# Kernel tuning notes

Hardware: AMD Instinct MI355X
Metric: run time of the kernel (lower is better)

The kernel has to match this reference:

```python
import jax, jax.numpy as jnp
import numpy as np

B, N, C = 8, 4096, 768
H = 12
D = C // H            # 64
BN = C // 2           # bottleneck dim 384
EPS_LN = 1e-5
EPS_ATTN = 1e-6


def layer_norm(x, g, b):
    mu = jnp.mean(x, axis=-1, keepdims=True)
    var = jnp.mean(jnp.square(x - mu), axis=-1, keepdims=True)
    return (x - mu) * jax.lax.rsqrt(var + EPS_LN) * g + b


def setup_inputs() -> dict:
    key = jax.random.key(0)
    ks = jax.random.split(key, 8)
    s = 0.02
    return {
        "x": jax.random.normal(ks[0], (B, N, C), jnp.float32),
        "w_qkv": jax.random.normal(ks[1], (C, 3 * C), jnp.float32) * s,
        "b_qkv": jnp.zeros((3 * C,), jnp.float32),
        "w_proj": jax.random.normal(ks[2], (C, C), jnp.float32) * s,
        "b_proj": jnp.zeros((C,), jnp.float32),
        "g1": jnp.ones((C,), jnp.float32),
        "beta1": jnp.zeros((C,), jnp.float32),
        "g2": jnp.ones((C,), jnp.float32),
        "beta2": jnp.zeros((C,), jnp.float32),
        "w_down": jax.random.normal(ks[3], (C, BN), jnp.float32) * s,
        "b_down": jnp.zeros((BN,), jnp.float32),
        "w_up": jax.random.normal(ks[4], (BN, C), jnp.float32) * s,
        "b_up": jnp.zeros((C,), jnp.float32),
        "g3": jnp.ones((C,), jnp.float32),
        "beta3": jnp.zeros((C,), jnp.float32),
    }


def _linear_attention(x, w_qkv, b_qkv, w_proj, b_proj):
    # x: (B, N, C)
    qkv = x @ w_qkv + b_qkv                       # (B, N, 3C)
    qkv = qkv.reshape(B, N, 3, H, D)
    qkv = jnp.transpose(qkv, (2, 0, 3, 1, 4))     # (3, B, H, N, D)
    q, k, v = qkv[0], qkv[1], qkv[2]
    fm = lambda t: jax.nn.elu(t) + 1.0            # positive feature map
    q, k = fm(q), fm(k)
    kv = jnp.einsum('bhnd,bhnv->bhdv', k, v)      # (B, H, D, D)
    out = jnp.einsum('bhnd,bhdv->bhnv', q, kv)    # (B, H, N, D)
    k_sum = k.sum(axis=2)                         # (B, H, D)
    normalizer = jnp.einsum('bhnd,bhd->bhn', q, k_sum) + EPS_ATTN
    out = out / normalizer[..., None]
    out = jnp.transpose(out, (0, 2, 1, 3)).reshape(B, N, C)
    return out @ w_proj + b_proj


def reference(x, w_qkv, b_qkv, w_proj, b_proj, g1, beta1, g2, beta2,
              w_down, b_down, w_up, b_up, g3, beta3):
    # DinomalyBlock forward (eval mode: dropout/noise disabled)
    x = x + _linear_attention(layer_norm(x, g1, beta1), w_qkv, b_qkv, w_proj, b_proj)
    r = layer_norm(x, g2, beta2)
    h = jax.nn.gelu(r @ w_down + b_down, approximate=False)  # torch GELU default = exact
    h = h @ w_up + b_up
    return layer_norm(r + h, g3, beta3)
```

## Files before the change

### kernel.cpp

```cpp
#include <hip/hip_runtime.h>
#include <hip/hip_bf16.h>
#include <cstdio>


typedef __attribute__((ext_vector_type(8))) short short8;
typedef __attribute__((ext_vector_type(4))) float floatx4;

__device__ __forceinline__ float bf2f(unsigned short u) {
    return __uint_as_float(((unsigned int)u) << 16);
}
__device__ __forceinline__ unsigned short f2bf(float f) {
    __hip_bfloat16 h = __float2bfloat16(f);
    return *reinterpret_cast<unsigned short*>(&h);
}

__device__ __forceinline__ void async_copy16(const unsigned short* g, unsigned short* l) {
    __builtin_amdgcn_global_load_lds(
        (const __attribute__((address_space(1))) unsigned int*)g,
        (__attribute__((address_space(3))) unsigned int*)l, 16, 0, 0);
}

__global__ __launch_bounds__(256) void transpose_all(
    const float* __restrict__ wq, const float* __restrict__ wp,
    const float* __restrict__ wd, const float* __restrict__ wu,
    unsigned short* __restrict__ tq, unsigned short* __restrict__ tp,
    unsigned short* __restrict__ td, unsigned short* __restrict__ tu)
{
    int blk = blockIdx.x;
    const float* w; unsigned short* o; int K, Nc, tx32;
    if (blk < 1728)      { w = wq; o = tq; K = 768; Nc = 2304; tx32 = 24; }
    else if (blk < 2304) { w = wp; o = tp; K = 768; Nc = 768;  tx32 = 24; blk -= 1728; }
    else if (blk < 2592) { w = wd; o = td; K = 768; Nc = 384;  tx32 = 24; blk -= 2304; }
    else                 { w = wu; o = tu; K = 384; Nc = 768;  tx32 = 12; blk -= 2592; }
    int kb = (blk % tx32) * 32, nb = (blk / tx32) * 32;
    __shared__ float tile[32][33];
    int tx = threadIdx.x & 31, ty = threadIdx.x >> 5;
    #pragma unroll
    for (int i = 0; i < 32; i += 8)
        tile[ty + i][tx] = w[(size_t)(kb + ty + i) * Nc + nb + tx];
    __syncthreads();
    #pragma unroll
    for (int i = 0; i < 32; i += 8)
        o[(size_t)(nb + ty + i) * K + kb + tx] = f2bf(tile[tx][ty + i]);
}

template<bool OBF16>
__global__ __launch_bounds__(384) void ln_kernel(
    const float* __restrict__ in, const float* __restrict__ gw,
    const float* __restrict__ bw, void* __restrict__ outp)
{
    int row = blockIdx.x;
    int t = threadIdx.x;
    float2 xv = ((const float2*)(in + (size_t)row * 768))[t];
    float s = xv.x + xv.y;
    float ss = xv.x * xv.x + xv.y * xv.y;
    #pragma unroll
    for (int o = 32; o > 0; o >>= 1) {
        s += __shfl_down(s, o);
        ss += __shfl_down(ss, o);
    }
    __shared__ float red[14];
    int wave = t >> 6, lane = t & 63;
    if (lane == 0) { red[wave] = s; red[6 + wave] = ss; }
    __syncthreads();
    if (t == 0) {
        float S = 0.f, SS = 0.f;
        #pragma unroll
        for (int i = 0; i < 6; i++) { S += red[i]; SS += red[6 + i]; }
        float mu = S * (1.0f / 768.0f);
        float var = SS * (1.0f / 768.0f) - mu * mu;
        red[12] = mu;
        red[13] = rsqrtf(var + 1e-5f);
    }
    __syncthreads();
    float mu = red[12], rstd = red[13];
    float2 g = ((const float2*)gw)[t];
    float2 b = ((const float2*)bw)[t];
    float y0 = (xv.x - mu) * rstd * g.x + b.x;
    float y1 = (xv.y - mu) * rstd * g.y + b.y;
    if (OBF16) {
        unsigned int pk = (unsigned int)f2bf(y0) | ((unsigned int)f2bf(y1) << 16);
        ((unsigned int*)outp)[(size_t)row * 384 + t] = pk;
    } else {
        ((float2*)outp)[(size_t)row * 384 + t] = make_float2(y0, y1);
    }
}

template<bool RES_F32, bool OUT_F32>
__global__ __launch_bounds__(384) void add_ln_kernel(
    const unsigned short* __restrict__ y, const void* __restrict__ resv,
    const float* __restrict__ gw, const float* __restrict__ bw,
    void* __restrict__ outp)
{
    int row = blockIdx.x;
    int t = threadIdx.x;
    unsigned int yp = ((const unsigned int*)(y + (size_t)row * 768))[t];
    float a0 = bf2f((unsigned short)(yp & 0xffff));
    float a1 = bf2f((unsigned short)(yp >> 16));
    float r0, r1;
    if (RES_F32) {
        float2 rv = ((const float2*)((const float*)resv + (size_t)row * 768))[t];
        r0 = rv.x; r1 = rv.y;
    } else {
        unsigned int rp = ((const unsigned int*)((const unsigned short*)resv + (size_t)row * 768))[t];
        r0 = bf2f((unsigned short)(rp & 0xffff));
        r1 = bf2f((unsigned short)(rp >> 16));
    }
    float v0 = a0 + r0, v1 = a1 + r1;
    float s = v0 + v1;
    float ss = v0 * v0 + v1 * v1;
    #pragma unroll
    for (int o = 32; o > 0; o >>= 1) {
        s += __shfl_down(s, o);
        ss += __shfl_down(ss, o);
    }
    __shared__ float red[14];
    int wave = t >> 6, lane = t & 63;
    if (lane == 0) { red[wave] = s; red[6 + wave] = ss; }
    __syncthreads();
    if (t == 0) {
        float S = 0.f, SS = 0.f;
        #pragma unroll
        for (int i = 0; i < 6; i++) { S += red[i]; SS += red[6 + i]; }
        float mu = S * (1.0f / 768.0f);
        float var = SS * (1.0f / 768.0f) - mu * mu;
        red[12] = mu;
        red[13] = rsqrtf(var + 1e-5f);
    }
    __syncthreads();
    float mu = red[12], rstd = red[13];
    float2 g = ((const float2*)gw)[t];
    float2 b = ((const float2*)bw)[t];
    float y0 = (v0 - mu) * rstd * g.x + b.x;
    float y1 = (v1 - mu) * rstd * g.y + b.y;
    if (OUT_F32) {
        ((float2*)outp)[(size_t)row * 384 + t] = make_float2(y0, y1);
    } else {
        unsigned int pk = (unsigned int)f2bf(y0) | ((unsigned int)f2bf(y1) << 16);
        ((unsigned int*)outp)[(size_t)row * 384 + t] = pk;
    }
}

template<int MODE>
__global__ __launch_bounds__(256, 4) void gemm_kernel(
    const unsigned short* __restrict__ A,
    const unsigned short* __restrict__ Wt,
    const float* __restrict__ bias,
    unsigned short* __restrict__ outp,
    int M, int K, int Nc)
{
    __shared__ __align__(16) unsigned short As[128][64];
    __shared__ __align__(16) unsigned short Bs[128][64];
    const int row0 = blockIdx.y * 128;
    const int col0 = blockIdx.x * 128;
    const int t = threadIdx.x;
    const int lane = t & 63;
    const int wave = t >> 6;
    const int wm = (wave >> 1) * 64;
    const int wn = (wave & 1) * 64;
    const int frow = lane & 15;
    const int quad = lane >> 4;
    const int lrow = lane >> 3;
    const int lchunk = (lane & 7) ^ lrow;

    floatx4 acc[4][4];
    #pragma unroll
    for (int i = 0; i < 4; i++)
        #pragma unroll
        for (int j = 0; j < 4; j++)
            acc[i][j] = (floatx4){0.f, 0.f, 0.f, 0.f};

    for (int k0 = 0; k0 < K; k0 += 64) {
        __syncthreads();
        #pragma unroll
        for (int q = 0; q < 4; q++) {
            int r = wave * 32 + q * 8 + lrow;
            async_copy16(A  + (size_t)(row0 + r) * K + k0 + lchunk * 8, &As[wave * 32 + q * 8][0]);
            async_copy16(Wt + (size_t)(col0 + r) * K + k0 + lchunk * 8, &Bs[wave * 32 + q * 8][0]);
        }
        __syncthreads();
        #pragma unroll
        for (int ks = 0; ks < 2; ks++) {
            const int pc = ((ks * 4 + quad) ^ (frow & 7)) * 8;
            short8 af[4], bf4[4];
            #pragma unroll
            for (int i = 0; i < 4; i++) af[i] = *(const short8*)&As[wm + i * 16 + frow][pc];
            #pragma unroll
            for (int j = 0; j < 4; j++) bf4[j] = *(const short8*)&Bs[wn + j * 16 + frow][pc];
            #pragma unroll
            for (int i = 0; i < 4; i++)
                #pragma unroll
                for (int j = 0; j < 4; j++)
                    acc[i][j] = __builtin_amdgcn_mfma_f32_16x16x32_bf16(
                        af[i], bf4[j], acc[i][j], 0, 0, 0);
        }
    }

    #pragma unroll
    for (int i = 0; i < 4; i++) {
        #pragma unroll
        for (int j = 0; j < 4; j++) {
            int col = col0 + wn + j * 16 + frow;
            float bcol = bias[col];
            #pragma unroll
            for (int rr = 0; rr < 4; rr++) {
                int row = row0 + wm + i * 16 + quad * 4 + rr;
                float v = acc[i][j][rr] + bcol;
                if (MODE == 0) {
                    if (col < 1536) v = (v > 0.f) ? (v + 1.f) : expf(v);
                } else if (MODE == 2) {
                    v = 0.5f * v * (1.0f + erff(v * 0.70710678118654752f));
                }
                outp[(size_t)row * Nc + col] = f2bf(v);
            }
        }
    }
}

__global__ __launch_bounds__(256) void kv_accum(
    const unsigned short* __restrict__ qkv, float* __restrict__ kvbuf)
{
    int blk = blockIdx.x;
    int chunk = blk & 7;
    int bh = blk >> 3;
    int b = bh / 12, h = bh % 12;
    int n0 = chunk * 512;
    int t = threadIdx.x;
    int d = t & 63, g = t >> 6;
    __shared__ float kl[2][32][68];
    __shared__ float vl[2][32][68];
    float kv[16];
    #pragma unroll
    for (int j = 0; j < 16; j++) kv[j] = 0.f;
    float ks = 0.f;

    int sr = t >> 3;
    int c16 = (t & 7) * 16;
    bool isk = c16 < 64;
    int cc = isk ? c16 : c16 - 64;
    const unsigned short* gbase =
        qkv + (size_t)(b * 4096 + n0 + sr) * 2304 + (isk ? 768 : 1536) + h * 64 + cc;
    uint4 r0, r1;
    auto loadg = [&](int nb) {
        const uint4* s = (const uint4*)(gbase + (size_t)nb * 2304);
        r0 = s[0]; r1 = s[1];
    };
    auto storel = [&](int buf) {
        float* dst = isk ? &kl[buf][sr][cc] : &vl[buf][sr][cc];
        const unsigned short* u0 = (const unsigned short*)&r0;
        const unsigned short* u1 = (const unsigned short*)&r1;
        #pragma unroll
        for (int i = 0; i < 8; i++) dst[i] = bf2f(u0[i]);
        #pragma unroll
        for (int i = 0; i < 8; i++) dst[8 + i] = bf2f(u1[i]);
    };

    loadg(0);
    storel(0);
    __syncthreads();
    for (int c = 0; c < 16; c++) {
        if (c < 15) loadg((c + 1) * 32);
        int bsel = c & 1;
        #pragma unroll 8
        for (int r2 = 0; r2 < 32; r2++) {
            float kd = kl[bsel][r2][d];
            ks += kd;
            const float4* vv = (const float4*)&vl[bsel][r2][g * 16];
            float4 a0 = vv[0], a1 = vv[1], a2 = vv[2], a3 = vv[3];
            kv[0]  += kd * a0.x; kv[1]  += kd * a0.y; kv[2]  += kd * a0.z; kv[3]  += kd * a0.w;
            kv[4]  += kd * a1.x; kv[5]  += kd * a1.y; kv[6]  += kd * a1.z; kv[7]  += kd * a1.w;
            kv[8]  += kd * a2.x; kv[9]  += kd * a2.y; kv[10] += kd * a2.z; kv[11] += kd * a2.w;
            kv[12] += kd * a3.x; kv[13] += kd * a3.y; kv[14] += kd * a3.z; kv[15] += kd * a3.w;
        }
        if (c < 15) storel((c + 1) & 1);
        __syncthreads();
    }
    float* dstg = kvbuf + (size_t)bh * 4160;
    #pragma unroll
    for (int j = 0; j < 16; j++)
        atomicAdd(&dstg[(g * 16 + j) * 64 + d], kv[j]);
    if (g == 0) atomicAdd(&dstg[4096 + d], ks);
}

__global__ __launch_bounds__(256) void attn_apply(
    const unsigned short* __restrict__ qkv, const float* __restrict__ kvbuf,
    unsigned short* __restrict__ attnC)
{
    int blk = blockIdx.x;
    int nchunk = blk & 31;
    int bh = blk >> 5;
    int b = bh / 12, h = bh % 12;
    int n0 = nchunk * 128;
    int t = threadIdx.x;
    int lane = t & 63, wave = t >> 6;
    __shared__ __align__(16) unsigned short ql[128][72];
    __shared__ __align__(16) unsigned short Bs[80][72];

    {
        const float* kvg = kvbuf + (size_t)bh * 4160;
        int e = t >> 2, d0 = (t & 3) * 16;
        const float4* src4 = (const float4*)(kvg + e * 64 + d0);
        #pragma unroll
        for (int i = 0; i < 4; i++) {
            float4 v = src4[i];
            unsigned long long pk = (unsigned long long)f2bf(v.x)
                | ((unsigned long long)f2bf(v.y) << 16)
                | ((unsigned long long)f2bf(v.z) << 32)
                | ((unsigned long long)f2bf(v.w) << 48);
            *(unsigned long long*)&Bs[e][d0 + i * 4] = pk;
        }
        if (t < 64) {
            Bs[64][t] = f2bf(kvg[4096 + t]);
            #pragma unroll
            for (int r = 65; r < 80; r++) Bs[r][t] = 0;
        }
    }
    {
        int r = t >> 1, c0 = (t & 1) * 32;
        const uint4* src = (const uint4*)(qkv + (size_t)(b * 4096 + n0 + r) * 2304 + h * 64 + c0);
        uint4* dst = (uint4*)&ql[r][c0];
        #pragma unroll
        for (int i = 0; i < 4; i++) dst[i] = src[i];
    }
    __syncthreads();

    int frow = lane & 15, quad = lane >> 4;
    floatx4 acc[2][5];
    #pragma unroll
    for (int it = 0; it < 2; it++)
        #pragma unroll
        for (int jt = 0; jt < 5; jt++)
            acc[it][jt] = (floatx4){0.f, 0.f, 0.f, 0.f};

    #pragma unroll
    for (int ks = 0; ks < 2; ks++) {
        int fk = ks * 32 + quad * 8;
        short8 a0 = *(const short8*)&ql[wave * 32 + frow][fk];
        short8 a1 = *(const short8*)&ql[wave * 32 + 16 + frow][fk];
        #pragma unroll
        for (int jt = 0; jt < 5; jt++) {
            short8 bb = *(const short8*)&Bs[jt * 16 + frow][fk];
            acc[0][jt] = __builtin_amdgcn_mfma_f32_16x16x32_bf16(a0, bb, acc[0][jt], 0, 0, 0);
            acc[1][jt] = __builtin_amdgcn_mfma_f32_16x16x32_bf16(a1, bb, acc[1][jt], 0, 0, 0);
        }
    }

    #pragma unroll
    for (int it = 0; it < 2; it++) {
        #pragma unroll
        for (int rr = 0; rr < 4; rr++) {
            float nv = __shfl(acc[it][4][rr], (lane & 48));
            float inv = 1.0f / (nv + 1e-6f);
            int row = n0 + wave * 32 + it * 16 + quad * 4 + rr;
            size_t obase = (size_t)(b * 4096 + row) * 768 + h * 64;
            #pragma unroll
            for (int jt = 0; jt < 4; jt++)
                attnC[obase + jt * 16 + frow] = f2bf(acc[it][jt][rr] * inv);
        }
    }
}

extern "C" void kernel_launch(void* const* d_in, const int* in_sizes, int n_in,
                              void* d_out, int out_size, void* d_ws, size_t ws_size,
                              hipStream_t stream)
{
    const float* x      = (const float*)d_in[0];
    const float* w_qkv  = (const float*)d_in[1];
    const float* b_qkv  = (const float*)d_in[2];
    const float* w_proj = (const float*)d_in[3];
    const float* b_proj = (const float*)d_in[4];
    const float* g1     = (const float*)d_in[5];
    const float* be1    = (const float*)d_in[6];
    const float* g2     = (const float*)d_in[7];
    const float* be2    = (const float*)d_in[8];
    const float* w_down = (const float*)d_in[9];
    const float* b_down = (const float*)d_in[10];
    const float* w_up   = (const float*)d_in[11];
    const float* b_up   = (const float*)d_in[12];
    const float* g3     = (const float*)d_in[13];
    const float* be3    = (const float*)d_in[14];

    char* p = (char*)d_ws;
    auto take = [&](size_t b) { char* q = p; p += (b + 255) & ~(size_t)255; return q; };
    unsigned short* wtq  = (unsigned short*)take((size_t)2304 * 768 * 2);
    unsigned short* wtp  = (unsigned short*)take((size_t)768 * 768 * 2);
    unsigned short* wtd  = (unsigned short*)take((size_t)384 * 768 * 2);
    unsigned short* wtu  = (unsigned short*)take((size_t)768 * 384 * 2);
    unsigned short* bufA = (unsigned short*)take((size_t)32768 * 768 * 2);
    unsigned short* qkvb = (unsigned short*)take((size_t)32768 * 2304 * 2);
    float*          kvb  = (float*)take((size_t)96 * 4160 * 4);
    unsigned short* hbuf = (unsigned short*)take((size_t)32768 * 384 * 2);
    unsigned short* rbuf    = qkvb;
    unsigned short* projout = qkvb + (size_t)32768 * 768;
    unsigned short* upout   = qkvb + (size_t)2 * 32768 * 768;

    size_t needed = (size_t)(p - (char*)d_ws);
    if (needed > ws_size)
        fprintf(stderr, "WARNING: ws too small: need %zu have %zu\n", needed, ws_size);

    transpose_all<<<2880, 256, 0, stream>>>(w_qkv, w_proj, w_down, w_up, wtq, wtp, wtd, wtu);
    hipMemsetAsync(kvb, 0, (size_t)96 * 4160 * 4, stream);

    ln_kernel<true><<<32768, 384, 0, stream>>>(x, g1, be1, bufA);
    gemm_kernel<0><<<dim3(18, 256), 256, 0, stream>>>(bufA, wtq, b_qkv, qkvb, 32768, 768, 2304);
    kv_accum<<<768, 256, 0, stream>>>(qkvb, kvb);
    attn_apply<<<3072, 256, 0, stream>>>(qkvb, kvb, bufA);
    gemm_kernel<1><<<dim3(6, 256), 256, 0, stream>>>(bufA, wtp, b_proj, projout, 32768, 768, 768);
    add_ln_kernel<true, false><<<32768, 384, 0, stream>>>(projout, x, g2, be2, rbuf);
    gemm_kernel<2><<<dim3(3, 256), 256, 0, stream>>>(rbuf, wtd, b_down, hbuf, 32768, 768, 384);
    gemm_kernel<1><<<dim3(6, 256), 256, 0, stream>>>(hbuf, wtu, b_up, upout, 32768, 384, 768);
    add_ln_kernel<false, true><<<32768, 384, 0, stream>>>(upout, rbuf, g3, be3, (float*)d_out);
}
```

Before: 712.5 us.

## Add 256x256-tile double-buffered MFMA GEMM for QKV, proj and up projections

Introduces a new 512-thread GEMM kernel that computes 256x256 output tiles with 8 waves, double-buffered LDS staging via async global-to-LDS copies, interleaved load/compute phases with explicit waitcnt and barriers, MFMA priority raising, and an XCD-aware block swizzle. It replaces the 128x128 GEMM for the QKV, attention projection and up projection, aiming to raise data reuse per tile and hide global load latency. Larger tiles increase register and LDS pressure and reduce the number of workgroups, and the hand-counted vmcnt waits must match the issued copies exactly.

```diff
diff --git a/kernel.cpp b/kernel.cpp
--- a/kernel.cpp
+++ b/kernel.cpp
@@ -18,6 +18,10 @@
     __builtin_amdgcn_global_load_lds(
         (const __attribute__((address_space(1))) unsigned int*)g,
         (__attribute__((address_space(3))) unsigned int*)l, 16, 0, 0);
+}
+
+__device__ __forceinline__ floatx4 MFMA16(short8 a, short8 b, floatx4 c) {
+    return __builtin_amdgcn_mfma_f32_16x16x32_bf16(a, b, c, 0, 0, 0);
 }
 
 __global__ __launch_bounds__(256) void transpose_all(
@@ -191,8 +195,7 @@
             for (int i = 0; i < 4; i++)
                 #pragma unroll
                 for (int j = 0; j < 4; j++)
-                    acc[i][j] = __builtin_amdgcn_mfma_f32_16x16x32_bf16(
-                        af[i], bf4[j], acc[i][j], 0, 0, 0);
+                    acc[i][j] = MFMA16(af[i], bf4[j], acc[i][j]);
         }
     }
 
@@ -205,6 +208,139 @@
             #pragma unroll
             for (int rr = 0; rr < 4; rr++) {
                 int row = row0 + wm + i * 16 + quad * 4 + rr;
+                float v = acc[i][j][rr] + bcol;
+                if (MODE == 0) {
+                    if (col < 1536) v = (v > 0.f) ? (v + 1.f) : expf(v);
+                } else if (MODE == 2) {
+                    v = 0.5f * v * (1.0f + erff(v * 0.70710678118654752f));
+                }
+                outp[(size_t)row * Nc + col] = f2bf(v);
+            }
+        }
+    }
+}
+
+template<int MODE>
+__global__ __launch_bounds__(512, 2) void gemm256(
+    const unsigned short* __restrict__ A,
+    const unsigned short* __restrict__ Wt,
+    const float* __restrict__ bias,
+    unsigned short* __restrict__ outp,
+    int M, int K, int Nc)
+{
+    __shared__ __align__(16) unsigned short As[2][2][256][32];
+    __shared__ __align__(16) unsigned short Bs[2][2][256][32];
+
+    const int gx = gridDim.x;
+    const int nwg = gx * gridDim.y;
+    const int lid = blockIdx.y * gx + blockIdx.x;
+    const int cpx = nwg >> 3;
+    const int swz = (lid & 7) * cpx + (lid >> 3);
+    const int row0 = (swz / gx) * 256;
+    const int col0 = (swz % gx) * 256;
+
+    const int t = threadIdx.x;
+    const int lane = t & 63;
+    const int wave = t >> 6;
+    const int wm = wave >> 2;
+    const int wn = wave & 3;
+    const int frow = lane & 15;
+    const int quad = lane >> 4;
+
+    const int srow = t >> 2;
+    const int gch = ((t & 3) ^ (srow & 3)) * 8;
+    const unsigned short* Ag = A  + (size_t)(row0 + srow) * K + gch;
+    const unsigned short* Bg = Wt + (size_t)(col0 + srow) * K + gch;
+    const size_t rstep = (size_t)128 * K;
+
+    const int nt = K >> 6;
+
+    floatx4 acc[8][4];
+    #pragma unroll
+    for (int i = 0; i < 8; i++)
+        #pragma unroll
+        for (int j = 0; j < 4; j++)
+            acc[i][j] = (floatx4){0.f, 0.f, 0.f, 0.f};
+    short8 af[4], bf[4];
+
+    auto stageA = [&](int slot, int ks, int tile) {
+        const unsigned short* g = Ag + (size_t)tile * 64 + ks * 32;
+        async_copy16(g,         &As[slot][ks][16 * wave][0]);
+        async_copy16(g + rstep, &As[slot][ks][128 + 16 * wave][0]);
+    };
+    auto stageB = [&](int slot, int ks, int tile) {
+        const unsigned short* g = Bg + (size_t)tile * 64 + ks * 32;
+        async_copy16(g,         &Bs[slot][ks][16 * wave][0]);
+        async_copy16(g + rstep, &Bs[slot][ks][128 + 16 * wave][0]);
+    };
+    const int pq = (quad ^ (frow & 3)) * 8;
+    auto ldA = [&](int slot, int ks, int ch) {
+        #pragma unroll
+        for (int ii = 0; ii < 4; ii++)
+            af[ii] = *(const short8*)&As[slot][ks][wm * 128 + (ch * 4 + ii) * 16 + frow][pq];
+    };
+    auto ldB = [&](int slot, int ks) {
+        #pragma unroll
+        for (int j = 0; j < 4; j++)
+            bf[j] = *(const short8*)&Bs[slot][ks][wn * 64 + j * 16 + frow][pq];
+    };
+    auto mm = [&](int ch) {
+        __builtin_amdgcn_s_setprio(1);
+        #pragma unroll
+        for (int ii = 0; ii < 4; ii++)
+            #pragma unroll
+            for (int j = 0; j < 4; j++)
+                acc[ch * 4 + ii][j] = MFMA16(af[ii], bf[j], acc[ch * 4 + ii][j]);
+        __builtin_amdgcn_s_setprio(0);
+    };
+
+    stageA(0, 0, 0); stageB(0, 0, 0);
+    stageA(0, 1, 0); stageB(0, 1, 0);
+    stageA(1, 0, 1); stageB(1, 0, 1);
+    asm volatile("s_waitcnt vmcnt(4)" ::: "memory");
+    __builtin_amdgcn_s_barrier();
+
+    for (int u = 0; u < nt; u++) {
+        const int sl = u & 1;
+        ldB(sl, 0); ldA(sl, 0, 0);
+        if (u + 1 < nt) stageA(sl ^ 1, 1, u + 1);
+        __builtin_amdgcn_s_barrier();
+        asm volatile("s_waitcnt lgkmcnt(0)" ::: "memory");
+        mm(0);
+        __builtin_amdgcn_s_barrier();
+        ldA(sl, 0, 1);
+        if (u + 1 < nt) stageB(sl ^ 1, 1, u + 1);
+        __builtin_amdgcn_s_barrier();
+        asm volatile("s_waitcnt lgkmcnt(0)" ::: "memory");
+        mm(1);
+        if (u + 1 < nt) asm volatile("s_waitcnt vmcnt(8)" ::: "memory");
+        else            asm volatile("s_waitcnt vmcnt(0)" ::: "memory");
+        __builtin_amdgcn_s_barrier();
+        ldB(sl, 1); ldA(sl, 1, 0);
+        if (u + 2 < nt) stageA(sl, 0, u + 2);
+        __builtin_amdgcn_s_barrier();
+        asm volatile("s_waitcnt lgkmcnt(0)" ::: "memory");
+        mm(0);
+        __builtin_amdgcn_s_barrier();
+        ldA(sl, 1, 1);
+        if (u + 2 < nt) stageB(sl, 0, u + 2);
+        __builtin_amdgcn_s_barrier();
+        asm volatile("s_waitcnt lgkmcnt(0)" ::: "memory");
+        mm(1);
+        if (u + 2 < nt) asm volatile("s_waitcnt vmcnt(8)" ::: "memory");
+        else            asm volatile("s_waitcnt vmcnt(0)" ::: "memory");
+        __builtin_amdgcn_s_barrier();
+    }
+
+    #pragma unroll
+    for (int i = 0; i < 8; i++) {
+        #pragma unroll
+        for (int j = 0; j < 4; j++) {
+            int col = col0 + wn * 64 + j * 16 + frow;
+            float bcol = bias[col];
+            #pragma unroll
+            for (int rr = 0; rr < 4; rr++) {
+                int row = row0 + wm * 128 + i * 16 + quad * 4 + rr;
                 float v = acc[i][j][rr] + bcol;
                 if (MODE == 0) {
                     if (col < 1536) v = (v > 0.f) ? (v + 1.f) : expf(v);
@@ -402,12 +538,12 @@
     hipMemsetAsync(kvb, 0, (size_t)96 * 4160 * 4, stream);
 
     ln_kernel<true><<<32768, 384, 0, stream>>>(x, g1, be1, bufA);
-    gemm_kernel<0><<<dim3(18, 256), 256, 0, stream>>>(bufA, wtq, b_qkv, qkvb, 32768, 768, 2304);
+    gemm256<0><<<dim3(9, 128), 512, 0, stream>>>(bufA, wtq, b_qkv, qkvb, 32768, 768, 2304);
     kv_accum<<<768, 256, 0, stream>>>(qkvb, kvb);
     attn_apply<<<3072, 256, 0, stream>>>(qkvb, kvb, bufA);
-    gemm_kernel<1><<<dim3(6, 256), 256, 0, stream>>>(bufA, wtp, b_proj, projout, 32768, 768, 768);
+    gemm256<1><<<dim3(3, 128), 512, 0, stream>>>(bufA, wtp, b_proj, projout, 32768, 768, 768);
     add_ln_kernel<true, false><<<32768, 384, 0, stream>>>(projout, x, g2, be2, rbuf);
     gemm_kernel<2><<<dim3(3, 256), 256, 0, stream>>>(rbuf, wtd, b_down, hbuf, 32768, 768, 384);
-    gemm_kernel<1><<<dim3(6, 256), 256, 0, stream>>>(hbuf, wtu, b_up, upout, 32768, 384, 768);
+    gemm256<1><<<dim3(3, 128), 512, 0, stream>>>(hbuf, wtu, b_up, upout, 32768, 384, 768);
     add_ln_kernel<false, true><<<32768, 384, 0, stream>>>(upout, rbuf, g3, be3, (float*)d_out);
 }
```

Result: slower. 742.1 us (+4.2%).

## Remap GEMM blocks per XCD for L2 reuse; single-buffer kv_accum LDS

Applied to the files above, without the earlier changes.

The GEMM kernel now remaps linear block IDs so that each of the 8 XCDs gets a contiguous band of row tiles, with column tiles grouped. The aim is better L2 reuse of A and W tiles within each chiplet. The kv_accum kernel drops its double-buffered LDS for a single buffer with an extra barrier per chunk and adds a launch-bounds occupancy hint of 4. This lowers LDS use so more blocks can run per CU, but it serialises the LDS store against compute. The remap assumes gridDim.y is divisible by 8 and that the group split covers all blocks.

```diff
diff --git a/kernel.cpp b/kernel.cpp
--- a/kernel.cpp
+++ b/kernel.cpp
@@ -18,6 +18,10 @@
     __builtin_amdgcn_global_load_lds(
         (const __attribute__((address_space(1))) unsigned int*)g,
         (__attribute__((address_space(3))) unsigned int*)l, 16, 0, 0);
+}
+
+__device__ __forceinline__ floatx4 MFMA16(short8 a, short8 b, floatx4 c) {
+    return __builtin_amdgcn_mfma_f32_16x16x32_bf16(a, b, c, 0, 0, 0);
 }
 
 __global__ __launch_bounds__(256) void transpose_all(
@@ -151,8 +155,25 @@
 {
     __shared__ __align__(16) unsigned short As[128][64];
     __shared__ __align__(16) unsigned short Bs[128][64];
-    const int row0 = blockIdx.y * 128;
-    const int col0 = blockIdx.x * 128;
+
+    const int gx = gridDim.x;
+    const int gy = gridDim.y;
+    int rb, cb;
+    {
+        const int lid = blockIdx.y * gx + blockIdx.x;
+        const int xcd = lid & 7;
+        const int o   = lid >> 3;
+        const int pry = gy >> 3;
+        const int cpg = (gx >= 12) ? (gx >> 1) : gx;
+        const int per = pry * cpg;
+        const int grp = o / per;
+        const int o2  = o - grp * per;
+        rb = xcd * pry + o2 / cpg;
+        cb = grp * cpg + o2 % cpg;
+    }
+    const int row0 = rb * 128;
+    const int col0 = cb * 128;
+
     const int t = threadIdx.x;
     const int lane = t & 63;
     const int wave = t >> 6;
@@ -191,8 +212,7 @@
             for (int i = 0; i < 4; i++)
                 #pragma unroll
                 for (int j = 0; j < 4; j++)
-                    acc[i][j] = __builtin_amdgcn_mfma_f32_16x16x32_bf16(
-                        af[i], bf4[j], acc[i][j], 0, 0, 0);
+                    acc[i][j] = MFMA16(af[i], bf4[j], acc[i][j]);
         }
     }
 
@@ -217,7 +237,7 @@
     }
 }
 
-__global__ __launch_bounds__(256) void kv_accum(
+__global__ __launch_bounds__(256, 4) void kv_accum(
     const unsigned short* __restrict__ qkv, float* __restrict__ kvbuf)
 {
     int blk = blockIdx.x;
@@ -227,8 +247,8 @@
     int n0 = chunk * 512;
     int t = threadIdx.x;
     int d = t & 63, g = t >> 6;
-    __shared__ float kl[2][32][68];
-    __shared__ float vl[2][32][68];
+    __shared__ float kl[32][68];
+    __shared__ float vl[32][68];
     float kv[16];
     #pragma unroll
     for (int j = 0; j < 16; j++) kv[j] = 0.f;
@@ -245,8 +265,8 @@
         const uint4* s = (const uint4*)(gbase + (size_t)nb * 2304);
         r0 = s[0]; r1 = s[1];
     };
-    auto storel = [&](int buf) {
-        float* dst = isk ? &kl[buf][sr][cc] : &vl[buf][sr][cc];
+    auto storel = [&]() {
+        float* dst = isk ? &kl[sr][cc] : &vl[sr][cc];
         const unsigned short* u0 = (const unsigned short*)&r0;
         const unsigned short* u1 = (const unsigned short*)&r1;
         #pragma unroll
@@ -256,23 +276,21 @@
     };
 
     loadg(0);
-    storel(0);
-    __syncthreads();
     for (int c = 0; c < 16; c++) {
+        storel();
+        __syncthreads();
         if (c < 15) loadg((c + 1) * 32);
-        int bsel = c & 1;
         #pragma unroll 8
         for (int r2 = 0; r2 < 32; r2++) {
-            float kd = kl[bsel][r2][d];
+            float kd = kl[r2][d];
             ks += kd;
-            const float4* vv = (const float4*)&vl[bsel][r2][g * 16];
+            const float4* vv = (const float4*)&vl[r2][g * 16];
             float4 a0 = vv[0], a1 = vv[1], a2 = vv[2], a3 = vv[3];
             kv[0]  += kd * a0.x; kv[1]  += kd * a0.y; kv[2]  += kd * a0.z; kv[3]  += kd * a0.w;
             kv[4]  += kd * a1.x; kv[5]  += kd * a1.y; kv[6]  += kd * a1.z; kv[7]  += kd * a1.w;
             kv[8]  += kd * a2.x; kv[9]  += kd * a2.y; kv[10] += kd * a2.z; kv[11] += kd * a2.w;
             kv[12] += kd * a3.x; kv[13] += kd * a3.y; kv[14] += kd * a3.z; kv[15] += kd * a3.w;
         }
-        if (c < 15) storel((c + 1) & 1);
         __syncthreads();
     }
     float* dstg = kvbuf + (size_t)bh * 4160;
```

After: 649.1 us. -8.9%, faster.
